# Kernel optimization log

Measured on AMD Instinct MI355X. Metric: run time of the kernel, lower is better.

Reference implementation:

```python
import jax, jax.numpy as jnp
import numpy as np

B, L, DM = 2, 1024, 1024
DI = 2 * DM          # expand=2
N = 16               # d_state
K = 4                # d_conv
DTR = DM // 16       # dt_rank = ceil(d_model/16) = 64
EPS = 1e-5


def setup_inputs() -> dict:
    key = jax.random.key(0)
    ks = jax.random.split(key, 8)
    s = lambda k, shape, sc=0.02: jax.random.normal(k, shape, jnp.float32) * sc
    return {
        "x": jax.random.normal(ks[0], (B, L, DM), jnp.float32),
        "ln_g": jnp.ones((DM,), jnp.float32),
        "ln_b": jnp.zeros((DM,), jnp.float32),
        "in_proj_w": s(ks[1], (2 * DI, DM)),
        "conv_w": s(ks[2], (DI, 1, K), 0.1),
        "conv_b": jnp.zeros((DI,), jnp.float32),
        "x_proj_w": s(ks[3], (DTR + 2 * N, DI)),
        "dt_proj_w": s(ks[4], (DI, DTR), 0.1),
        "dt_proj_b": s(ks[5], (DI,), 0.5),
        "A_log": jnp.log(jnp.tile(jnp.arange(1, N + 1, dtype=jnp.float32), (DI, 1))),
        "D": jnp.ones((DI,), jnp.float32),
        "out_proj_w": s(ks[6], (DM, DI)),
    }


def reference(x, ln_g, ln_b, in_proj_w, conv_w, conv_b, x_proj_w,
              dt_proj_w, dt_proj_b, A_log, D, out_proj_w):
    residual = x
    # LayerNorm
    mu = x.mean(-1, keepdims=True)
    var = ((x - mu) ** 2).mean(-1, keepdims=True)
    xn = (x - mu) * jax.lax.rsqrt(var + EPS) * ln_g + ln_b
    # in_proj -> (x, z)
    xz = jnp.einsum('bld,ed->ble', xn, in_proj_w)   # (B,L,2*DI)
    xi, z = jnp.split(xz, 2, axis=-1)
    # depthwise causal conv1d + SiLU
    xc = jax.lax.conv_general_dilated(
        xi.transpose(0, 2, 1), conv_w, (1,), [(K - 1, 0)],
        feature_group_count=DI, dimension_numbers=('NCH', 'OIH', 'NCH'))
    u = jax.nn.silu((xc + conv_b[None, :, None]).transpose(0, 2, 1))  # (B,L,DI)
    # x_proj -> dt, B, C
    xdbl = jnp.einsum('bld,ed->ble', u, x_proj_w)
    dt, Bc, Cc = jnp.split(xdbl, [DTR, DTR + N], axis=-1)
    delta = jax.nn.softplus(jnp.einsum('blr,dr->bld', dt, dt_proj_w) + dt_proj_b)
    A = -jnp.exp(A_log)                              # (DI,N)
    dA = jnp.exp(delta[..., None] * A)               # (B,L,DI,N)
    dBu = delta[..., None] * Bc[:, :, None, :] * u[..., None]

    def step(h, inp):
        dA_t, dBu_t, C_t = inp                        # (B,DI,N),(B,DI,N),(B,N)
        h = dA_t * h + dBu_t
        y = jnp.einsum('bdn,bn->bd', h, C_t)
        return h, y

    h0 = jnp.zeros((B, DI, N), x.dtype)
    _, ys = jax.lax.scan(step, h0, (dA.transpose(1, 0, 2, 3),
                                    dBu.transpose(1, 0, 2, 3),
                                    Cc.transpose(1, 0, 2)))
    y = ys.transpose(1, 0, 2) + u * D                # (B,L,DI)
    y = y * jax.nn.silu(z)
    out = jnp.einsum('bld,ed->ble', y, out_proj_w)
    return residual + out
```

## Files before the change

### kernel.cpp

```cpp
#include <hip/hip_runtime.h>
#include <hip/hip_bf16.h>
#include <math.h>

#define B_   2
#define L_   1024
#define DM_  1024
#define DI_  2048
#define NS_  16
#define DTR_ 64
#define M_   (B_ * L_)
#define XZW_ (2 * DI_)
#define XDW_ 128
#define CH_  32
#define CLEN_ (L_ / CH_)
#define SK_  8
#define KCH_ (DI_ / SK_)

typedef __attribute__((ext_vector_type(8))) short bf16x8;
typedef __attribute__((ext_vector_type(4))) float f32x4;
typedef __attribute__((ext_vector_type(4))) unsigned short u16x4;

static __device__ __forceinline__ unsigned short f2bf(float f) {
  __hip_bfloat16 h = __float2bfloat16(f);
  return *reinterpret_cast<unsigned short*>(&h);
}
static __device__ __forceinline__ float bf2f(unsigned short u) {
  unsigned int x = ((unsigned int)u) << 16;
  float f;
  __builtin_memcpy(&f, &x, 4);
  return f;
}

__global__ __launch_bounds__(256) void ln_kernel(
    const float* __restrict__ x, const float* __restrict__ g,
    const float* __restrict__ b, unsigned short* __restrict__ xnb)
{
  int r = blockIdx.x;
  int t = threadIdx.x;
  const float4* xr = (const float4*)(x + (size_t)r * DM_);
  float4 v = xr[t];
  float s  = v.x + v.y + v.z + v.w;
  float ss = v.x * v.x + v.y * v.y + v.z * v.z + v.w * v.w;
  for (int m = 32; m >= 1; m >>= 1) {
    s  += __shfl_down(s, m);
    ss += __shfl_down(ss, m);
  }
  __shared__ float sb[4], ssb[4];
  int w = t >> 6, lane = t & 63;
  if (lane == 0) { sb[w] = s; ssb[w] = ss; }
  __syncthreads();
  s  = sb[0] + sb[1] + sb[2] + sb[3];
  ss = ssb[0] + ssb[1] + ssb[2] + ssb[3];
  float mu  = s * (1.f / DM_);
  float var = ss * (1.f / DM_) - mu * mu;
  float rs  = rsqrtf(var + 1e-5f);
  float4 gv = ((const float4*)g)[t];
  float4 bv = ((const float4*)b)[t];
  u16x4 o;
  o[0] = f2bf((v.x - mu) * rs * gv.x + bv.x);
  o[1] = f2bf((v.y - mu) * rs * gv.y + bv.y);
  o[2] = f2bf((v.z - mu) * rs * gv.z + bv.z);
  o[3] = f2bf((v.w - mu) * rs * gv.w + bv.w);
  ((u16x4*)xnb)[r * 256 + t] = o;
}

__global__ __launch_bounds__(256) void f2bf_kernel(
    const float4* __restrict__ in, u16x4* __restrict__ outp)
{
  int i = blockIdx.x * 256 + threadIdx.x;
  float4 v = in[i];
  u16x4 o;
  o[0] = f2bf(v.x); o[1] = f2bf(v.y); o[2] = f2bf(v.z); o[3] = f2bf(v.w);
  outp[i] = o;
}

template<int MODE, int TN>
__global__ __launch_bounds__(256) void gemm_mfma(
    const short* __restrict__ A, int lda,
    const short* __restrict__ Bw, int ldb,
    float* __restrict__ C, int ldc, int Kdim,
    const float* __restrict__ res, int ldres)
{
  constexpr int MREP = (TN == 128) ? 4 : 2;
  constexpr int NREP = 4;
  constexpr int WM   = (TN == 128) ? 64 : 32;
  __shared__ __align__(16) short As[2][128 * 64];
  __shared__ __align__(16) short Bs[2][TN * 64];
  const int bm = blockIdx.y * 128, bn = blockIdx.x * TN;
  const int t = threadIdx.x, wid = t >> 6, lane = t & 63;
  const int wr = (TN == 128) ? (wid >> 1) : wid;
  const int wc = (TN == 128) ? (wid & 1) : 0;

  f32x4 acc[MREP][NREP];
#pragma unroll
  for (int i = 0; i < MREP; ++i)
#pragma unroll
    for (int j = 0; j < NREP; ++j) acc[i][j] = (f32x4){0.f, 0.f, 0.f, 0.f};

  const int srow = wid * 8 + (lane >> 3);
  const int sc   = lane & 7;
  const int r16 = lane & 15, khalf = lane >> 4;

  auto STAGE = [&](int buf, int k0) {
#pragma unroll
    for (int q = 0; q < 4; ++q) {
      int row = q * 32 + srow;
      int csw = sc ^ (row & 7);
      const short* gA = A + (size_t)(bm + row) * lda + k0 + csw * 8;
      __builtin_amdgcn_global_load_lds(
          (const __attribute__((address_space(1))) void*)gA,
          (__attribute__((address_space(3))) void*)(&As[buf][q * 2048 + wid * 512]),
          16, 0, 0);
    }
#pragma unroll
    for (int q = 0; q < TN / 32; ++q) {
      int row = q * 32 + srow;
      int csw = sc ^ (row & 7);
      const short* gB = Bw + (size_t)(bn + row) * ldb + k0 + csw * 8;
      __builtin_amdgcn_global_load_lds(
          (const __attribute__((address_space(1))) void*)gB,
          (__attribute__((address_space(3))) void*)(&Bs[buf][q * 2048 + wid * 512]),
          16, 0, 0);
    }
  };

  const int nt = Kdim >> 6;
  STAGE(0, 0);
  int cur = 0;
  for (int ti = 0; ti < nt; ++ti) {
    __syncthreads();
    if (ti + 1 < nt) STAGE(cur ^ 1, (ti + 1) << 6);

    bf16x8 af[MREP][2], bfr[NREP][2];
#pragma unroll
    for (int m = 0; m < MREP; ++m)
#pragma unroll
      for (int kk = 0; kk < 2; ++kk) {
        int c16 = kk * 4 + khalf;
        int rowa = wr * WM + m * 16 + r16;
        af[m][kk] = *(const bf16x8*)(&As[cur][rowa * 64 + ((c16 ^ (rowa & 7)) << 3)]);
      }
#pragma unroll
    for (int nn = 0; nn < NREP; ++nn)
#pragma unroll
      for (int kk = 0; kk < 2; ++kk) {
        int c16 = kk * 4 + khalf;
        int rowb = wc * 64 + nn * 16 + r16;
        bfr[nn][kk] = *(const bf16x8*)(&Bs[cur][rowb * 64 + ((c16 ^ (rowb & 7)) << 3)]);
      }
#pragma unroll
    for (int kk = 0; kk < 2; ++kk)
#pragma unroll
      for (int m = 0; m < MREP; ++m)
#pragma unroll
        for (int nn = 0; nn < NREP; ++nn)
          acc[m][nn] = __builtin_amdgcn_mfma_f32_16x16x32_bf16(
              af[m][kk], bfr[nn][kk], acc[m][nn], 0, 0, 0);
    cur ^= 1;
  }

  const int rgrp = lane >> 4;
#pragma unroll
  for (int m = 0; m < MREP; ++m)
#pragma unroll
    for (int nn = 0; nn < NREP; ++nn) {
      int col = bn + wc * 64 + nn * 16 + r16;
#pragma unroll
      for (int rg = 0; rg < 4; ++rg) {
        int row = bm + wr * WM + m * 16 + rgrp * 4 + rg;
        float v = acc[m][nn][rg];
        if (MODE == 2) v += res[(size_t)row * ldres + col];
        C[(size_t)row * ldc + col] = v;
      }
    }
}

#define BM 64
#define BN 64
#define BK 32
#define PADR 68

__global__ __launch_bounds__(256) void gemm_nt(
    const float* __restrict__ A, int lda,
    const float* __restrict__ Bw, int ldb,
    float* __restrict__ C, int ldc,
    int Mrows, int Ncols, int Kdim,
    int mode, const float* __restrict__ bias)
{
  __shared__ float as[BK][PADR];
  __shared__ float bs[BK][PADR];
  int bm = blockIdx.y * BM;
  int bn = blockIdx.x * BN;
  int t  = threadIdx.x;
  int tx = t & 15, ty = t >> 4;

  float acc[4][4] = {};

  int m0 = t >> 3;
  int kq = t & 7;
  const float4 z4 = {0.f, 0.f, 0.f, 0.f};

  for (int k0 = 0; k0 < Kdim; k0 += BK) {
    float4 a0 = *(const float4*)(A + (size_t)(bm + m0) * lda + k0 + kq * 4);
    float4 a1 = *(const float4*)(A + (size_t)(bm + m0 + 32) * lda + k0 + kq * 4);
    float4 b0 = (bn + m0 < Ncols)
        ? *(const float4*)(Bw + (size_t)(bn + m0) * ldb + k0 + kq * 4) : z4;
    float4 b1 = (bn + m0 + 32 < Ncols)
        ? *(const float4*)(Bw + (size_t)(bn + m0 + 32) * ldb + k0 + kq * 4) : z4;
    as[kq * 4 + 0][m0] = a0.x;  as[kq * 4 + 1][m0] = a0.y;
    as[kq * 4 + 2][m0] = a0.z;  as[kq * 4 + 3][m0] = a0.w;
    as[kq * 4 + 0][m0 + 32] = a1.x;  as[kq * 4 + 1][m0 + 32] = a1.y;
    as[kq * 4 + 2][m0 + 32] = a1.z;  as[kq * 4 + 3][m0 + 32] = a1.w;
    bs[kq * 4 + 0][m0] = b0.x;  bs[kq * 4 + 1][m0] = b0.y;
    bs[kq * 4 + 2][m0] = b0.z;  bs[kq * 4 + 3][m0] = b0.w;
    bs[kq * 4 + 0][m0 + 32] = b1.x;  bs[kq * 4 + 1][m0 + 32] = b1.y;
    bs[kq * 4 + 2][m0 + 32] = b1.z;  bs[kq * 4 + 3][m0 + 32] = b1.w;
    __syncthreads();

#pragma unroll
    for (int kk = 0; kk < BK; ++kk) {
      float4 a4 = *(const float4*)&as[kk][ty * 4];
      float4 b4 = *(const float4*)&bs[kk][tx * 4];
      float ar[4] = {a4.x, a4.y, a4.z, a4.w};
      float br[4] = {b4.x, b4.y, b4.z, b4.w};
#pragma unroll
      for (int i = 0; i < 4; ++i)
#pragma unroll
        for (int j = 0; j < 4; ++j)
          acc[i][j] = fmaf(ar[i], br[j], acc[i][j]);
    }
    __syncthreads();
  }

#pragma unroll
  for (int i = 0; i < 4; ++i) {
    int r = bm + ty * 4 + i;
    int c = bn + tx * 4;
    float vv[4];
#pragma unroll
    for (int j = 0; j < 4; ++j) {
      float v = acc[i][j];
      if (mode == 1) {
        v += bias[c + j];
        v = (v > 20.f) ? v : log1pf(expf(v));
      }
      vv[j] = v;
    }
    float4 o = {vv[0], vv[1], vv[2], vv[3]};
    *(float4*)(C + (size_t)r * ldc + c) = o;
  }
}

__global__ __launch_bounds__(256) void gemm_nt_sk(
    const float* __restrict__ A, int lda,
    const float* __restrict__ Bw, int ldb,
    float* __restrict__ part, int Ncols)
{
  __shared__ float as[BK][PADR];
  __shared__ float bs[BK][PADR];
  int bm = blockIdx.y * BM;
  int bn = blockIdx.x * BN;
  int sk = blockIdx.z;
  int t  = threadIdx.x;
  int tx = t & 15, ty = t >> 4;

  float acc[4][4] = {};

  int m0 = t >> 3;
  int kq = t & 7;
  const float4 z4 = {0.f, 0.f, 0.f, 0.f};

  for (int k0 = sk * KCH_; k0 < (sk + 1) * KCH_; k0 += BK) {
    float4 a0 = *(const float4*)(A + (size_t)(bm + m0) * lda + k0 + kq * 4);
    float4 a1 = *(const float4*)(A + (size_t)(bm + m0 + 32) * lda + k0 + kq * 4);
    float4 b0 = (bn + m0 < Ncols)
        ? *(const float4*)(Bw + (size_t)(bn + m0) * ldb + k0 + kq * 4) : z4;
    float4 b1 = (bn + m0 + 32 < Ncols)
        ? *(const float4*)(Bw + (size_t)(bn + m0 + 32) * ldb + k0 + kq * 4) : z4;
    as[kq * 4 + 0][m0] = a0.x;  as[kq * 4 + 1][m0] = a0.y;
    as[kq * 4 + 2][m0] = a0.z;  as[kq * 4 + 3][m0] = a0.w;
    as[kq * 4 + 0][m0 + 32] = a1.x;  as[kq * 4 + 1][m0 + 32] = a1.y;
    as[kq * 4 + 2][m0 + 32] = a1.z;  as[kq * 4 + 3][m0 + 32] = a1.w;
    bs[kq * 4 + 0][m0] = b0.x;  bs[kq * 4 + 1][m0] = b0.y;
    bs[kq * 4 + 2][m0] = b0.z;  bs[kq * 4 + 3][m0] = b0.w;
    bs[kq * 4 + 0][m0 + 32] = b1.x;  bs[kq * 4 + 1][m0 + 32] = b1.y;
    bs[kq * 4 + 2][m0 + 32] = b1.z;  bs[kq * 4 + 3][m0 + 32] = b1.w;
    __syncthreads();

#pragma unroll
    for (int kk = 0; kk < BK; ++kk) {
      float4 a4 = *(const float4*)&as[kk][ty * 4];
      float4 b4 = *(const float4*)&bs[kk][tx * 4];
      float ar[4] = {a4.x, a4.y, a4.z, a4.w};
      float br[4] = {b4.x, b4.y, b4.z, b4.w};
#pragma unroll
      for (int i = 0; i < 4; ++i)
#pragma unroll
        for (int j = 0; j < 4; ++j)
          acc[i][j] = fmaf(ar[i], br[j], acc[i][j]);
    }
    __syncthreads();
  }

  float* outp = part + (size_t)sk * M_ * XDW_;
#pragma unroll
  for (int i = 0; i < 4; ++i) {
    int r = bm + ty * 4 + i;
    int c = bn + tx * 4;
    float4 o = {acc[i][0], acc[i][1], acc[i][2], acc[i][3]};
    *(float4*)(outp + (size_t)r * XDW_ + c) = o;
  }
}

__global__ __launch_bounds__(256) void reduce_sk(
    const float* __restrict__ part, float* __restrict__ xdbl)
{
  int i = blockIdx.x * 256 + threadIdx.x;
  float s = 0.f;
#pragma unroll
  for (int sk = 0; sk < SK_; ++sk) s += part[(size_t)sk * M_ * XDW_ + i];
  xdbl[i] = s;
}

#define LCH 32
__global__ __launch_bounds__(256) void conv_silu_kernel(
    const float* __restrict__ xz, const float* __restrict__ cw,
    const float* __restrict__ cb, float* __restrict__ u)
{
  int d  = blockIdx.x * 256 + threadIdx.x;
  int l0 = blockIdx.y * LCH;
  int b  = blockIdx.z;
  float w0 = cw[d * 4 + 0], w1 = cw[d * 4 + 1];
  float w2 = cw[d * 4 + 2], w3 = cw[d * 4 + 3];
  float bias = cb[d];
  const float* xi = xz + (size_t)(b * L_) * XZW_ + d;
  float x3 = (l0 >= 3) ? xi[(size_t)(l0 - 3) * XZW_] : 0.f;
  float x2 = (l0 >= 2) ? xi[(size_t)(l0 - 2) * XZW_] : 0.f;
  float x1 = (l0 >= 1) ? xi[(size_t)(l0 - 1) * XZW_] : 0.f;
  for (int l = l0; l < l0 + LCH; ++l) {
    float x0 = xi[(size_t)l * XZW_];
    float v = w0 * x3 + w1 * x2 + w2 * x1 + w3 * x0 + bias;
    float uu = v / (1.f + __expf(-v));
    u[((size_t)(b * L_) + l) * DI_ + d] = uu;
    x3 = x2; x2 = x1; x1 = x0;
  }
}

__global__ __launch_bounds__(256) void scan_p1(
    const float* __restrict__ dlt, const float* __restrict__ u,
    const float* __restrict__ xdbl, const float* __restrict__ A_log,
    float* __restrict__ Pbuf, unsigned short* __restrict__ hend)
{
  int t = threadIdx.x;
  int ng = t & 3, dl = t >> 2;
  int d = blockIdx.x * 64 + dl;
  int b = blockIdx.y;
  int c = blockIdx.z;
  int l0 = c * CLEN_;
  float4 Al = *(const float4*)(A_log + d * NS_ + ng * 4);
  float A0 = -__expf(Al.x), A1 = -__expf(Al.y), A2 = -__expf(Al.z), A3 = -__expf(Al.w);
  float h0 = 0.f, h1 = 0.f, h2 = 0.f, h3 = 0.f, S = 0.f;
  const float* dp = dlt + ((size_t)(b * L_) + l0) * DI_ + d;
  const float* up = u   + ((size_t)(b * L_) + l0) * DI_ + d;
  const float* xp = xdbl + ((size_t)(b * L_) + l0) * XDW_ + DTR_ + ng * 4;
  float dv = dp[0], uv = up[0];
  float4 Bv = *(const float4*)xp;
  for (int l = 0; l < CLEN_; ++l) {
    int ln = (l + 1 < CLEN_) ? l + 1 : l;
    float dv_n = dp[(size_t)ln * DI_];
    float uv_n = up[(size_t)ln * DI_];
    float4 Bv_n = *(const float4*)(xp + (size_t)ln * XDW_);
    float dvu = dv * uv;
    h0 = __expf(dv * A0) * h0 + dvu * Bv.x;
    h1 = __expf(dv * A1) * h1 + dvu * Bv.y;
    h2 = __expf(dv * A2) * h2 + dvu * Bv.z;
    h3 = __expf(dv * A3) * h3 + dvu * Bv.w;
    S += dv;
    dv = dv_n; uv = uv_n; Bv = Bv_n;
  }
  size_t i = ((size_t)((b * CH_ + c) * DI_) + d) * NS_ + ng * 4;
  float4 P; P.x = __expf(S * A0); P.y = __expf(S * A1);
  P.z = __expf(S * A2); P.w = __expf(S * A3);
  u16x4 H; H[0] = f2bf(h0); H[1] = f2bf(h1); H[2] = f2bf(h2); H[3] = f2bf(h3);
  *(float4*)(Pbuf + i) = P;
  *(u16x4*)(hend + i) = H;
}

__global__ __launch_bounds__(256) void scan_p2(
    float* __restrict__ Pbuf, const unsigned short* __restrict__ hend)
{
  int tid = blockIdx.x * 256 + threadIdx.x;
  int n = tid & 15;
  int d = (tid >> 4) & (DI_ - 1);
  int b = tid >> 15;
  float h = 0.f;
  for (int c = 0; c < CH_; ++c) {
    size_t i = ((size_t)((b * CH_ + c) * DI_) + d) * NS_ + n;
    float Pv = Pbuf[i];
    float he = bf2f(hend[i]);
    Pbuf[i] = h;
    h = Pv * h + he;
  }
}

__global__ __launch_bounds__(256) void scan_p3(
    const float* __restrict__ dlt, const float* __restrict__ u,
    const float* __restrict__ xdbl, const float* __restrict__ A_log,
    const float* __restrict__ hin, const float* __restrict__ xz,
    const float* __restrict__ Dp, unsigned short* __restrict__ yb)
{
  int t = threadIdx.x;
  int ng = t & 3, dl = t >> 2;
  int d = blockIdx.x * 64 + dl;
  int b = blockIdx.y;
  int c = blockIdx.z;
  int l0 = c * CLEN_;
  float4 Al = *(const float4*)(A_log + d * NS_ + ng * 4);
  float A0 = -__expf(Al.x), A1 = -__expf(Al.y), A2 = -__expf(Al.z), A3 = -__expf(Al.w);
  size_t i0 = ((size_t)((b * CH_ + c) * DI_) + d) * NS_ + ng * 4;
  float4 hv = *(const float4*)(hin + i0);
  float h0 = hv.x, h1 = hv.y, h2 = hv.z, h3 = hv.w;
  float Dd = Dp[d];
  const float* dp = dlt + ((size_t)(b * L_) + l0) * DI_ + d;
  const float* up = u   + ((size_t)(b * L_) + l0) * DI_ + d;
  const float* xp = xdbl + ((size_t)(b * L_) + l0) * XDW_ + DTR_ + ng * 4;
  const float* zp = xz + ((size_t)(b * L_) + l0) * XZW_ + DI_ + d;
  unsigned short* yp = yb + ((size_t)(b * L_) + l0) * DI_ + d;
  float dv = dp[0], uv = up[0];
  float4 Bv = *(const float4*)xp;
  float4 Cv = *(const float4*)(xp + NS_);
  for (int l = 0; l < CLEN_; ++l) {
    int ln = (l + 1 < CLEN_) ? l + 1 : l;
    float dv_n = dp[(size_t)ln * DI_];
    float uv_n = up[(size_t)ln * DI_];
    float4 Bv_n = *(const float4*)(xp + (size_t)ln * XDW_);
    float4 Cv_n = *(const float4*)(xp + (size_t)ln * XDW_ + NS_);
    float dvu = dv * uv;
    h0 = __expf(dv * A0) * h0 + dvu * Bv.x;
    h1 = __expf(dv * A1) * h1 + dvu * Bv.y;
    h2 = __expf(dv * A2) * h2 + dvu * Bv.z;
    h3 = __expf(dv * A3) * h3 + dvu * Bv.w;
    float py = h0 * Cv.x + h1 * Cv.y + h2 * Cv.z + h3 * Cv.w;
    py += __shfl_xor(py, 1);
    py += __shfl_xor(py, 2);
    if (ng == 0) {
      float z = zp[(size_t)l * XZW_];
      float zs = z / (1.f + __expf(-z));
      yp[(size_t)l * DI_] = f2bf((py + uv * Dd) * zs);
    }
    dv = dv_n; uv = uv_n; Bv = Bv_n; Cv = Cv_n;
  }
}

extern "C" void kernel_launch(void* const* d_in, const int* in_sizes, int n_in,
                              void* d_out, int out_size, void* d_ws, size_t ws_size,
                              hipStream_t stream)
{
  const float* x         = (const float*)d_in[0];
  const float* ln_g      = (const float*)d_in[1];
  const float* ln_b      = (const float*)d_in[2];
  const float* in_proj_w = (const float*)d_in[3];
  const float* conv_w    = (const float*)d_in[4];
  const float* conv_b    = (const float*)d_in[5];
  const float* x_proj_w  = (const float*)d_in[6];
  const float* dt_proj_w = (const float*)d_in[7];
  const float* dt_proj_b = (const float*)d_in[8];
  const float* A_log     = (const float*)d_in[9];
  const float* Dp        = (const float*)d_in[10];
  const float* out_proj_w= (const float*)d_in[11];
  float* out = (float*)d_out;

  float* ws = (float*)d_ws;
  float* xz   = ws;
  float* u    = ws + 8388608;
  float* xdbl = ws + 12582912;
  float* dlt  = ws + 12845056;
  unsigned short* xnb   = (unsigned short*)(ws + 17039360);
  float* winb_f = ws + 18087936;
  unsigned short* winb  = (unsigned short*)winb_f;
  unsigned short* woutb = (unsigned short*)(ws + 20185088);
  unsigned short* yb    = (unsigned short*)(ws + 21233664);
  float* Pbuf = winb_f;
  unsigned short* hendb = xnb;

  ln_kernel<<<M_, 256, 0, stream>>>(x, ln_g, ln_b, xnb);

  f2bf_kernel<<<4096, 256, 0, stream>>>((const float4*)in_proj_w, (u16x4*)winb);
  f2bf_kernel<<<2048, 256, 0, stream>>>((const float4*)out_proj_w, (u16x4*)woutb);

  gemm_mfma<0, 128><<<dim3(XZW_ / 128, M_ / 128), 256, 0, stream>>>(
      (const short*)xnb, DM_, (const short*)winb, DM_, xz, XZW_, DM_, nullptr, 0);

  conv_silu_kernel<<<dim3(DI_ / 256, L_ / LCH, B_), 256, 0, stream>>>(
      xz, conv_w, conv_b, u);

  gemm_nt_sk<<<dim3(XDW_ / BN, M_ / BM, SK_), 256, 0, stream>>>(
      u, DI_, x_proj_w, DI_, winb_f, 96);
  reduce_sk<<<(M_ * XDW_) / 256, 256, 0, stream>>>(winb_f, xdbl);

  gemm_nt<<<dim3(DI_ / BN, M_ / BM), 256, 0, stream>>>(
      xdbl, XDW_, dt_proj_w, DTR_, dlt, DI_, M_, DI_, DTR_, 1, dt_proj_b);

  scan_p1<<<dim3(DI_ / 64, B_, CH_), 256, 0, stream>>>(dlt, u, xdbl, A_log, Pbuf, hendb);
  scan_p2<<<(B_ * DI_ * NS_) / 256, 256, 0, stream>>>(Pbuf, hendb);
  scan_p3<<<dim3(DI_ / 64, B_, CH_), 256, 0, stream>>>(
      dlt, u, xdbl, A_log, Pbuf, xz, Dp, yb);

  gemm_mfma<2, 64><<<dim3(DM_ / 64, M_ / 128), 256, 0, stream>>>(
      (const short*)yb, DI_, (const short*)woutb, DI_, out, DM_, DI_, x, DM_);
}
```

Baseline: 273.3 us.

## Store xz in bf16 and move dt_proj onto MFMA bf16 GEMM

```diff
diff --git a/kernel.cpp b/kernel.cpp
--- a/kernel.cpp
+++ b/kernel.cpp
@@ -78,8 +78,9 @@
 __global__ __launch_bounds__(256) void gemm_mfma(
     const short* __restrict__ A, int lda,
     const short* __restrict__ Bw, int ldb,
-    float* __restrict__ C, int ldc, int Kdim,
-    const float* __restrict__ res, int ldres)
+    void* __restrict__ Cv, int ldc, int Kdim,
+    const float* __restrict__ res, int ldres,
+    const float* __restrict__ bias)
 {
   constexpr int MREP = (TN == 128) ? 4 : 2;
   constexpr int NREP = 4;
@@ -169,8 +170,15 @@
       for (int rg = 0; rg < 4; ++rg) {
         int row = bm + wr * WM + m * 16 + rgrp * 4 + rg;
         float v = acc[m][nn][rg];
+        if (MODE == 1) {
+          v += bias[col];
+          v = (v > 20.f) ? v : log1pf(expf(v));
+        }
         if (MODE == 2) v += res[(size_t)row * ldres + col];
-        C[(size_t)row * ldc + col] = v;
+        if (MODE == 3)
+          ((unsigned short*)Cv)[(size_t)row * ldc + col] = f2bf(v);
+        else
+          ((float*)Cv)[(size_t)row * ldc + col] = v;
       }
     }
 }
@@ -179,77 +187,6 @@
 #define BN 64
 #define BK 32
 #define PADR 68
-
-__global__ __launch_bounds__(256) void gemm_nt(
-    const float* __restrict__ A, int lda,
-    const float* __restrict__ Bw, int ldb,
-    float* __restrict__ C, int ldc,
-    int Mrows, int Ncols, int Kdim,
-    int mode, const float* __restrict__ bias)
-{
-  __shared__ float as[BK][PADR];
-  __shared__ float bs[BK][PADR];
-  int bm = blockIdx.y * BM;
-  int bn = blockIdx.x * BN;
-  int t  = threadIdx.x;
-  int tx = t & 15, ty = t >> 4;
-
-  float acc[4][4] = {};
-
-  int m0 = t >> 3;
-  int kq = t & 7;
-  const float4 z4 = {0.f, 0.f, 0.f, 0.f};
-
-  for (int k0 = 0; k0 < Kdim; k0 += BK) {
-    float4 a0 = *(const float4*)(A + (size_t)(bm + m0) * lda + k0 + kq * 4);
-    float4 a1 = *(const float4*)(A + (size_t)(bm + m0 + 32) * lda + k0 + kq * 4);
-    float4 b0 = (bn + m0 < Ncols)
-        ? *(const float4*)(Bw + (size_t)(bn + m0) * ldb + k0 + kq * 4) : z4;
-    float4 b1 = (bn + m0 + 32 < Ncols)
-        ? *(const float4*)(Bw + (size_t)(bn + m0 + 32) * ldb + k0 + kq * 4) : z4;
-    as[kq * 4 + 0][m0] = a0.x;  as[kq * 4 + 1][m0] = a0.y;
-    as[kq * 4 + 2][m0] = a0.z;  as[kq * 4 + 3][m0] = a0.w;
-    as[kq * 4 + 0][m0 + 32] = a1.x;  as[kq * 4 + 1][m0 + 32] = a1.y;
-    as[kq * 4 + 2][m0 + 32] = a1.z;  as[kq * 4 + 3][m0 + 32] = a1.w;
-    bs[kq * 4 + 0][m0] = b0.x;  bs[kq * 4 + 1][m0] = b0.y;
-    bs[kq * 4 + 2][m0] = b0.z;  bs[kq * 4 + 3][m0] = b0.w;
-    bs[kq * 4 + 0][m0 + 32] = b1.x;  bs[kq * 4 + 1][m0 + 32] = b1.y;
-    bs[kq * 4 + 2][m0 + 32] = b1.z;  bs[kq * 4 + 3][m0 + 32] = b1.w;
-    __syncthreads();
-
-#pragma unroll
-    for (int kk = 0; kk < BK; ++kk) {
-      float4 a4 = *(const float4*)&as[kk][ty * 4];
-      float4 b4 = *(const float4*)&bs[kk][tx * 4];
-      float ar[4] = {a4.x, a4.y, a4.z, a4.w};
-      float br[4] = {b4.x, b4.y, b4.z, b4.w};
-#pragma unroll
-      for (int i = 0; i < 4; ++i)
-#pragma unroll
-        for (int j = 0; j < 4; ++j)
-          acc[i][j] = fmaf(ar[i], br[j], acc[i][j]);
-    }
-    __syncthreads();
-  }
-
-#pragma unroll
-  for (int i = 0; i < 4; ++i) {
-    int r = bm + ty * 4 + i;
-    int c = bn + tx * 4;
-    float vv[4];
-#pragma unroll
-    for (int j = 0; j < 4; ++j) {
-      float v = acc[i][j];
-      if (mode == 1) {
-        v += bias[c + j];
-        v = (v > 20.f) ? v : log1pf(expf(v));
-      }
-      vv[j] = v;
-    }
-    float4 o = {vv[0], vv[1], vv[2], vv[3]};
-    *(float4*)(C + (size_t)r * ldc + c) = o;
-  }
-}
 
 __global__ __launch_bounds__(256) void gemm_nt_sk(
     const float* __restrict__ A, int lda,
@@ -313,18 +250,21 @@
 }
 
 __global__ __launch_bounds__(256) void reduce_sk(
-    const float* __restrict__ part, float* __restrict__ xdbl)
+    const float* __restrict__ part, float* __restrict__ xdbl,
+    unsigned short* __restrict__ xdtb)
 {
   int i = blockIdx.x * 256 + threadIdx.x;
   float s = 0.f;
 #pragma unroll
   for (int sk = 0; sk < SK_; ++sk) s += part[(size_t)sk * M_ * XDW_ + i];
   xdbl[i] = s;
-}
-
-#define LCH 32
+  int col = i & (XDW_ - 1);
+  if (col < DTR_) xdtb[(size_t)(i >> 7) * DTR_ + col] = f2bf(s);
+}
+
+#define LCH 8
 __global__ __launch_bounds__(256) void conv_silu_kernel(
-    const float* __restrict__ xz, const float* __restrict__ cw,
+    const unsigned short* __restrict__ xzb, const float* __restrict__ cw,
     const float* __restrict__ cb, float* __restrict__ u)
 {
   int d  = blockIdx.x * 256 + threadIdx.x;
@@ -333,12 +273,13 @@
   float w0 = cw[d * 4 + 0], w1 = cw[d * 4 + 1];
   float w2 = cw[d * 4 + 2], w3 = cw[d * 4 + 3];
   float bias = cb[d];
-  const float* xi = xz + (size_t)(b * L_) * XZW_ + d;
-  float x3 = (l0 >= 3) ? xi[(size_t)(l0 - 3) * XZW_] : 0.f;
-  float x2 = (l0 >= 2) ? xi[(size_t)(l0 - 2) * XZW_] : 0.f;
-  float x1 = (l0 >= 1) ? xi[(size_t)(l0 - 1) * XZW_] : 0.f;
+  const unsigned short* xi = xzb + (size_t)(b * L_) * XZW_ + d;
+  float x3 = (l0 >= 3) ? bf2f(xi[(size_t)(l0 - 3) * XZW_]) : 0.f;
+  float x2 = (l0 >= 2) ? bf2f(xi[(size_t)(l0 - 2) * XZW_]) : 0.f;
+  float x1 = (l0 >= 1) ? bf2f(xi[(size_t)(l0 - 1) * XZW_]) : 0.f;
+#pragma unroll
   for (int l = l0; l < l0 + LCH; ++l) {
-    float x0 = xi[(size_t)l * XZW_];
+    float x0 = bf2f(xi[(size_t)l * XZW_]);
     float v = w0 * x3 + w1 * x2 + w2 * x1 + w3 * x0 + bias;
     float uu = v / (1.f + __expf(-v));
     u[((size_t)(b * L_) + l) * DI_ + d] = uu;
@@ -406,7 +347,7 @@
 __global__ __launch_bounds__(256) void scan_p3(
     const float* __restrict__ dlt, const float* __restrict__ u,
     const float* __restrict__ xdbl, const float* __restrict__ A_log,
-    const float* __restrict__ hin, const float* __restrict__ xz,
+    const float* __restrict__ hin, const unsigned short* __restrict__ xzb,
     const float* __restrict__ Dp, unsigned short* __restrict__ yb)
 {
   int t = threadIdx.x;
@@ -424,7 +365,7 @@
   const float* dp = dlt + ((size_t)(b * L_) + l0) * DI_ + d;
   const float* up = u   + ((size_t)(b * L_) + l0) * DI_ + d;
   const float* xp = xdbl + ((size_t)(b * L_) + l0) * XDW_ + DTR_ + ng * 4;
-  const float* zp = xz + ((size_t)(b * L_) + l0) * XZW_ + DI_ + d;
+  const unsigned short* zp = xzb + ((size_t)(b * L_) + l0) * XZW_ + DI_ + d;
   unsigned short* yp = yb + ((size_t)(b * L_) + l0) * DI_ + d;
   float dv = dp[0], uv = up[0];
   float4 Bv = *(const float4*)xp;
@@ -444,7 +385,7 @@
     py += __shfl_xor(py, 1);
     py += __shfl_xor(py, 2);
     if (ng == 0) {
-      float z = zp[(size_t)l * XZW_];
+      float z = bf2f(zp[(size_t)l * XZW_]);
       float zs = z / (1.f + __expf(-z));
       yp[(size_t)l * DI_] = f2bf((py + uv * Dd) * zs);
     }
@@ -471,15 +412,17 @@
   float* out = (float*)d_out;
 
   float* ws = (float*)d_ws;
-  float* xz   = ws;
-  float* u    = ws + 8388608;
-  float* xdbl = ws + 12582912;
-  float* dlt  = ws + 12845056;
-  unsigned short* xnb   = (unsigned short*)(ws + 17039360);
-  float* winb_f = ws + 18087936;
+  unsigned short* xzb = (unsigned short*)ws;
+  float* u    = ws + 4194304;
+  float* xdbl = ws + 8388608;
+  float* dlt  = ws + 8650752;
+  unsigned short* xdtb = (unsigned short*)(ws + 12845056);
+  unsigned short* dtwb = (unsigned short*)(ws + 12910592);
+  unsigned short* xnb  = (unsigned short*)(ws + 12976128);
+  float* winb_f = ws + 14024704;
   unsigned short* winb  = (unsigned short*)winb_f;
-  unsigned short* woutb = (unsigned short*)(ws + 20185088);
-  unsigned short* yb    = (unsigned short*)(ws + 21233664);
+  unsigned short* woutb = (unsigned short*)(ws + 16121856);
+  unsigned short* yb    = (unsigned short*)(ws + 17170432);
   float* Pbuf = winb_f;
   unsigned short* hendb = xnb;
 
@@ -487,25 +430,28 @@
 
   f2bf_kernel<<<4096, 256, 0, stream>>>((const float4*)in_proj_w, (u16x4*)winb);
   f2bf_kernel<<<2048, 256, 0, stream>>>((const float4*)out_proj_w, (u16x4*)woutb);
-
-  gemm_mfma<0, 128><<<dim3(XZW_ / 128, M_ / 128), 256, 0, stream>>>(
-      (const short*)xnb, DM_, (const short*)winb, DM_, xz, XZW_, DM_, nullptr, 0);
+  f2bf_kernel<<<128, 256, 0, stream>>>((const float4*)dt_proj_w, (u16x4*)dtwb);
+
+  gemm_mfma<3, 128><<<dim3(XZW_ / 128, M_ / 128), 256, 0, stream>>>(
+      (const short*)xnb, DM_, (const short*)winb, DM_, xzb, XZW_, DM_,
+      nullptr, 0, nullptr);
 
   conv_silu_kernel<<<dim3(DI_ / 256, L_ / LCH, B_), 256, 0, stream>>>(
-      xz, conv_w, conv_b, u);
+      xzb, conv_w, conv_b, u);
 
   gemm_nt_sk<<<dim3(XDW_ / BN, M_ / BM, SK_), 256, 0, stream>>>(
       u, DI_, x_proj_w, DI_, winb_f, 96);
-  reduce_sk<<<(M_ * XDW_) / 256, 256, 0, stream>>>(winb_f, xdbl);
-
-  gemm_nt<<<dim3(DI_ / BN, M_ / BM), 256, 0, stream>>>(
-      xdbl, XDW_, dt_proj_w, DTR_, dlt, DI_, M_, DI_, DTR_, 1, dt_proj_b);
+  reduce_sk<<<(M_ * XDW_) / 256, 256, 0, stream>>>(winb_f, xdbl, xdtb);
+
+  gemm_mfma<1, 128><<<dim3(DI_ / 128, M_ / 128), 256, 0, stream>>>(
+      (const short*)xdtb, DTR_, (const short*)dtwb, DTR_, dlt, DI_, DTR_,
+      nullptr, 0, dt_proj_b);
 
   scan_p1<<<dim3(DI_ / 64, B_, CH_), 256, 0, stream>>>(dlt, u, xdbl, A_log, Pbuf, hendb);
   scan_p2<<<(B_ * DI_ * NS_) / 256, 256, 0, stream>>>(Pbuf, hendb);
   scan_p3<<<dim3(DI_ / 64, B_, CH_), 256, 0, stream>>>(
-      dlt, u, xdbl, A_log, Pbuf, xz, Dp, yb);
+      dlt, u, xdbl, A_log, Pbuf, xzb, Dp, yb);
 
   gemm_mfma<2, 64><<<dim3(DM_ / 64, M_ / 128), 256, 0, stream>>>(
-      (const short*)yb, DI_, (const short*)woutb, DI_, out, DM_, DI_, x, DM_);
-}
+      (const short*)yb, DI_, (const short*)woutb, DI_, out, DM_, DI_, x, DM_, nullptr);
+}
```

Measured after the change: 271.5 us. Within noise of the previous version (-0.7%).
